# Kernel optimization log

Hardware: AMD Instinct MI355X
Metric: run time of the kernel (lower is better)

The kernel has to match this reference:

```python
import jax, jax.numpy as jnp
import numpy as np

N = 50000   # nodes
E = 800000  # edges
V = 10000   # vocab
D = 128     # emb_dim
H = 128     # hidden_dim
C = 10      # num_classes
G = 512     # graphs in batch


def setup_inputs() -> dict:
    key = jax.random.key(0)
    ks = jax.random.split(key, 10)
    return {
        "x_tokens": jax.random.randint(ks[0], (N,), 0, V),
        "edge_index": jax.random.randint(ks[1], (2, E), 0, N),
        "batch": jnp.sort(jax.random.randint(ks[2], (N,), 0, G)),
        "emb": jax.random.normal(ks[3], (V, D), dtype=jnp.float32) * 0.05,
        "w1": jax.random.normal(ks[4], (D, H), dtype=jnp.float32) * 0.05,
        "b1": jax.random.normal(ks[5], (H,), dtype=jnp.float32) * 0.05,
        "w2": jax.random.normal(ks[6], (H, H), dtype=jnp.float32) * 0.05,
        "b2": jax.random.normal(ks[7], (H,), dtype=jnp.float32) * 0.05,
        "lin_w": jax.random.normal(ks[8], (H, C), dtype=jnp.float32) * 0.05,
        "lin_b": jax.random.normal(ks[9], (C,), dtype=jnp.float32) * 0.05,
    }


def _gcn_conv(x, W, b, src, dst, norm):
    # PyG GCNConv: x' = D^{-1/2}(A+I)D^{-1/2} X W + b (self-loops already in src/dst)
    h = x @ W                                  # [N, H]
    msg = h[src] * norm[:, None]               # [E+N, H] gather + scale
    return jax.ops.segment_sum(msg, dst, num_segments=N) + b


def reference(x_tokens, edge_index, batch, emb, w1, b1, w2, b2, lin_w, lin_b):
    # embedding with padding_idx=0 (row 0 forced to zero)
    table = emb * (jnp.arange(V) != 0)[:, None].astype(emb.dtype)
    x = table[x_tokens]                        # [N, D]

    # add self loops, symmetric degree normalization (computed once)
    loops = jnp.arange(N)
    src = jnp.concatenate([edge_index[0], loops])
    dst = jnp.concatenate([edge_index[1], loops])
    deg = jax.ops.segment_sum(jnp.ones_like(dst, dtype=x.dtype), dst, num_segments=N)
    dis = jax.lax.rsqrt(deg)                   # deg >= 1 due to self loops
    norm = dis[src] * dis[dst]                 # [E+N]

    x = jax.nn.relu(_gcn_conv(x, w1, b1, src, dst, norm))
    x = jax.nn.relu(_gcn_conv(x, w2, b2, src, dst, norm))

    # global mean pool over graphs
    sums = jax.ops.segment_sum(x, batch, num_segments=G)          # [G, H]
    cnts = jax.ops.segment_sum(jnp.ones((N,), x.dtype), batch, num_segments=G)
    pooled = sums / jnp.maximum(cnts, 1.0)[:, None]

    return pooled @ lin_w + lin_b              # [G, C]
```

## Files before the change

### kernel.cpp

```cpp
#include <hip/hip_runtime.h>
#include <hip/hip_bf16.h>


typedef unsigned int uint;
typedef unsigned short ushort;
typedef __attribute__((ext_vector_type(8))) short bf16x8;
typedef __attribute__((ext_vector_type(4))) float f32x4;

__device__ inline float bf_lo(uint u) { return __uint_as_float(u << 16); }
__device__ inline float bf_hi(uint u) { return __uint_as_float(u & 0xffff0000u); }
__device__ inline ushort f2bf(float f) {
    uint u = __float_as_uint(f);
    return (ushort)((u + 0x7fffu + ((u >> 16) & 1u)) >> 16);
}
__device__ inline uint pack2bf(float a, float b) {
    return (uint)f2bf(a) | ((uint)f2bf(b) << 16);
}

#define EPB 2048
#define CAP 8192

__global__ __launch_bounds__(256) void init0(int* __restrict__ bcur,
                                             const float* __restrict__ W1,
                                             const float* __restrict__ W2,
                                             ushort* __restrict__ W1t,
                                             ushort* __restrict__ W2t) {
    if (blockIdx.x == 0) {
        bcur[threadIdx.x] = 0;
    } else {
        int i = (blockIdx.x - 1) * 256 + threadIdx.x;
        const float* Ws = (i < 16384) ? W1 : W2;
        ushort* Wd      = (i < 16384) ? W1t : W2t;
        int j = i & 16383;
        int nn = j >> 7, k = j & 127;
        Wd[j] = f2bf(Ws[k * 128 + nn]);
    }
}

__device__ void scatter_body(int* lds,
                             const int* __restrict__ src,
                             const int* __restrict__ dst,
                             int* __restrict__ bcur,
                             uint* __restrict__ bstage,
                             int E, int NB, int bid) {
    int*  lh    = lds;
    int*  lbase = lds + 256;
    int*  gbase = lds + 513;
    int*  lcur  = lds + 769;
    int*  ls    = lds + 1025;
    uint* stage = (uint*)(lds + 1284);
    const int t = threadIdx.x;
    const int base = bid * EPB;
    const int end  = min(E, base + EPB);
    const int tot  = end - base;

    lh[t] = 0;
    __syncthreads();

    uint pk[8]; int bk[8]; int cnt = 0;
    for (int i = base + t; i < end; i += 256) {
        int s = src[i];
        uint d = (uint)dst[i];
        bk[cnt] = (int)(d >> 8);
        pk[cnt] = (uint)s | ((d & 255u) << 24);
        atomicAdd(&lh[bk[cnt]], 1);
        ++cnt;
    }
    __syncthreads();

    if (t < NB && lh[t]) gbase[t] = t * CAP + atomicAdd(&bcur[t], lh[t]);
    {
        int v = lh[t];
        ls[t] = v;
        __syncthreads();
        for (int off = 1; off < 256; off <<= 1) {
            int x = (t >= off) ? ls[t - off] : 0;
            __syncthreads();
            ls[t] += x;
            __syncthreads();
        }
        lbase[t] = ls[t] - v;
        if (t == 255) lbase[256] = ls[255];
        lcur[t] = 0;
    }
    __syncthreads();

    for (int j = 0; j < cnt; ++j) {
        int p = lbase[bk[j]] + atomicAdd(&lcur[bk[j]], 1);
        stage[p] = pk[j];
    }
    __syncthreads();

    for (int i = t; i < tot; i += 256) {
        int lo = 0, hi = 256;
        while (lo + 1 < hi) {
            int mid = (lo + hi) >> 1;
            if (lbase[mid] <= i) lo = mid; else hi = mid;
        }
        bstage[gbase[lo] + (i - lbase[lo])] = stage[i];
    }
}

__device__ void csr_body(int* lds,
                         const uint* __restrict__ bstage,
                         const int* __restrict__ bcur,
                         float* __restrict__ dis,
                         int* __restrict__ rbeg,
                         int* __restrict__ rend,
                         int* __restrict__ csr,
                         int N, int b) {
    int* lh    = lds;
    int* ls    = lds + 256;
    int* lbase = lds + 512;
    int* lcur  = lds + 768;
    const int t = threadIdx.x;
    const int base  = b * CAP;
    const int cntb  = bcur[b];
    const int n0    = b << 8;
    const int nn    = min(256, N - n0);

    lh[t] = 0;
    __syncthreads();
    for (int i = t; i < cntb; i += 256)
        atomicAdd(&lh[bstage[base + i] >> 24], 1);
    __syncthreads();

    const int v = lh[t];
    ls[t] = v;
    __syncthreads();
    for (int off = 1; off < 256; off <<= 1) {
        int x = (t >= off) ? ls[t - off] : 0;
        __syncthreads();
        ls[t] += x;
        __syncthreads();
    }
    lbase[t] = ls[t] - v;
    lcur[t] = 0;
    if (t < nn) {
        dis[n0 + t]  = rsqrtf((float)v + 1.0f);
        rbeg[n0 + t] = base + lbase[t];
        rend[n0 + t] = base + lbase[t] + v;
    }
    __syncthreads();

    for (int i = t; i < cntb; i += 256) {
        uint e = bstage[base + i];
        int dl = (int)(e >> 24);
        int pos = base + lbase[dl] + atomicAdd(&lcur[dl], 1);
        csr[pos] = (int)(e & 0xFFFFFFu);
    }
}

template<bool GATHER, bool SCALE>
__device__ void gemm_body(ushort* wl,
                          const ushort* __restrict__ Xbf,
                          const int* __restrict__ tokens,
                          const float* __restrict__ emb,
                          const ushort* __restrict__ Wt,
                          const float* __restrict__ dis,
                          ushort* __restrict__ Out, int n, int bid) {
    const int tid = threadIdx.x;
    {
        const int row  = tid >> 1;
        const int half = tid & 1;
        const int base = row * 256 + half * 128;
#pragma unroll
        for (int i = 0; i < 8; ++i) {
            int off = base + i * 16;
            uint4 v = *(const uint4*)((const char*)Wt + off);
            int swz = off ^ ((row & 7) << 4);
            *(uint4*)((char*)wl + swz) = v;
        }
    }
    __syncthreads();

    const int w  = tid >> 6;
    const int l  = tid & 63;
    const int lr = l & 15;
    const int lg = l >> 4;
    const int rowBase = bid * 128 + w * 32;

    f32x4 acc[2][8];
#pragma unroll
    for (int s = 0; s < 2; ++s)
#pragma unroll
        for (int ct = 0; ct < 8; ++ct) acc[s][ct] = (f32x4){0.f, 0.f, 0.f, 0.f};

    bf16x8 afrag[2][4];
#pragma unroll
    for (int s = 0; s < 2; ++s) {
        const int row = rowBase + s * 16 + lr;
        if (row < n) {
            if (GATHER) {
                const int tok = tokens[row];
                if (tok != 0) {
                    const float* ep = emb + (size_t)tok * 128;
#pragma unroll
                    for (int kk = 0; kk < 4; ++kk) {
                        const float* q = ep + kk * 32 + lg * 8;
                        float4 lo = *(const float4*)q;
                        float4 hi = *(const float4*)(q + 4);
                        uint4 pk;
                        pk.x = pack2bf(lo.x, lo.y); pk.y = pack2bf(lo.z, lo.w);
                        pk.z = pack2bf(hi.x, hi.y); pk.w = pack2bf(hi.z, hi.w);
                        union { uint4 u; bf16x8 b; } c; c.u = pk;
                        afrag[s][kk] = c.b;
                    }
                } else {
#pragma unroll
                    for (int kk = 0; kk < 4; ++kk) afrag[s][kk] = (bf16x8){0,0,0,0,0,0,0,0};
                }
            } else {
                const ushort* xp = Xbf + (size_t)row * 128;
#pragma unroll
                for (int kk = 0; kk < 4; ++kk)
                    afrag[s][kk] = *(const bf16x8*)(xp + kk * 32 + lg * 8);
            }
        } else {
#pragma unroll
            for (int kk = 0; kk < 4; ++kk) afrag[s][kk] = (bf16x8){0,0,0,0,0,0,0,0};
        }
    }

#pragma unroll
    for (int ct = 0; ct < 8; ++ct) {
#pragma unroll
        for (int kk = 0; kk < 4; ++kk) {
            const int nrow = ct * 16 + lr;
            int off = nrow * 256 + kk * 64 + lg * 16;
            off ^= ((nrow & 7) << 4);
            bf16x8 b = *(const bf16x8*)((const char*)wl + off);
            acc[0][ct] = __builtin_amdgcn_mfma_f32_16x16x32_bf16(afrag[0][kk], b, acc[0][ct], 0, 0, 0);
            acc[1][ct] = __builtin_amdgcn_mfma_f32_16x16x32_bf16(afrag[1][kk], b, acc[1][ct], 0, 0, 0);
        }
    }

#pragma unroll
    for (int s = 0; s < 2; ++s) {
#pragma unroll
        for (int r = 0; r < 4; ++r) {
            const int row = rowBase + s * 16 + lg * 4 + r;
            if (row < n) {
                const float sc = SCALE ? dis[row] : 1.0f;
                ushort* op = Out + (size_t)row * 128 + lr;
#pragma unroll
                for (int ct = 0; ct < 8; ++ct)
                    op[ct * 16] = f2bf(acc[s][ct][r] * sc);
            }
        }
    }
}

__global__ __launch_bounds__(256) void scatter_gemm1_fused(const int* __restrict__ src,
                                                           const int* __restrict__ dst,
                                                           int* __restrict__ bcur,
                                                           uint* __restrict__ bstage,
                                                           const int* __restrict__ tokens,
                                                           const float* __restrict__ emb,
                                                           const ushort* __restrict__ W1t,
                                                           ushort* __restrict__ H,
                                                           int E, int NB, int EB, int N) {
    __shared__ ushort wl[128 * 128];
    const int b = blockIdx.x;
    if (b < EB) {
        scatter_body((int*)wl, src, dst, bcur, bstage, E, NB, b);
    } else {
        gemm_body<true, false>(wl, nullptr, tokens, emb, W1t, nullptr, H, N, b - EB);
    }
}

__global__ __launch_bounds__(256) void csr_poolz(const uint* __restrict__ bstage,
                                                 const int* __restrict__ bcur,
                                                 float* __restrict__ dis,
                                                 int* __restrict__ rbeg,
                                                 int* __restrict__ rend,
                                                 int* __restrict__ csr,
                                                 int4* __restrict__ poolz, int pz4,
                                                 int N, int NB) {
    __shared__ int lds[1024];
    const int b = blockIdx.x;
    if (b < NB) {
        csr_body(lds, bstage, bcur, dis, rbeg, rend, csr, N, b);
    } else {
        int i = (b - NB) * 256 + threadIdx.x;
        if (i < pz4) poolz[i] = make_int4(0, 0, 0, 0);
    }
}

__global__ __launch_bounds__(256) void gemm2_kernel(const ushort* __restrict__ Xbf,
                                                    const ushort* __restrict__ Wt,
                                                    const float* __restrict__ dis,
                                                    ushort* __restrict__ Out, int n) {
    __shared__ ushort wl[128 * 128];
    gemm_body<false, true>(wl, Xbf, nullptr, nullptr, Wt, dis, Out, n, blockIdx.x);
}

__global__ __launch_bounds__(256) void aggregate_w(const ushort* __restrict__ H,
                                                   const float* __restrict__ dis,
                                                   const int* __restrict__ rbeg,
                                                   const int* __restrict__ rend,
                                                   const int* __restrict__ csr,
                                                   const float* __restrict__ bias,
                                                   ushort* __restrict__ Out, int n) {
    const int g = threadIdx.x >> 4;
    const int l = threadIdx.x & 15;
    const int node = blockIdx.x * 16 + g;
    if (node >= n) return;

    const float dn = dis[node];
    const uint4 hq = *(const uint4*)(H + (size_t)node * 128 + l * 8);
    const int e0 = rbeg[node];
    const int e1 = rend[node];

    float s0_=0.f,s1_=0.f,s2_=0.f,s3_=0.f,s4_=0.f,s5_=0.f,s6_=0.f,s7_=0.f;

    int e = e0;
    for (; e + 8 <= e1; e += 8) {
        int a[8];
#pragma unroll
        for (int j = 0; j < 8; ++j) a[j] = csr[e + j];
        float w[8];
#pragma unroll
        for (int j = 0; j < 8; ++j) w[j] = dis[a[j]];
        uint4 h[8];
#pragma unroll
        for (int j = 0; j < 8; ++j) h[j] = *(const uint4*)(H + (size_t)a[j] * 128 + l * 8);
#pragma unroll
        for (int j = 0; j < 8; ++j) {
            s0_ += bf_lo(h[j].x) * w[j]; s1_ += bf_hi(h[j].x) * w[j];
            s2_ += bf_lo(h[j].y) * w[j]; s3_ += bf_hi(h[j].y) * w[j];
            s4_ += bf_lo(h[j].z) * w[j]; s5_ += bf_hi(h[j].z) * w[j];
            s6_ += bf_lo(h[j].w) * w[j]; s7_ += bf_hi(h[j].w) * w[j];
        }
    }
    for (; e + 4 <= e1; e += 4) {
        int a[4];
#pragma unroll
        for (int j = 0; j < 4; ++j) a[j] = csr[e + j];
        float w[4];
#pragma unroll
        for (int j = 0; j < 4; ++j) w[j] = dis[a[j]];
        uint4 h[4];
#pragma unroll
        for (int j = 0; j < 4; ++j) h[j] = *(const uint4*)(H + (size_t)a[j] * 128 + l * 8);
#pragma unroll
        for (int j = 0; j < 4; ++j) {
            s0_ += bf_lo(h[j].x) * w[j]; s1_ += bf_hi(h[j].x) * w[j];
            s2_ += bf_lo(h[j].y) * w[j]; s3_ += bf_hi(h[j].y) * w[j];
            s4_ += bf_lo(h[j].z) * w[j]; s5_ += bf_hi(h[j].z) * w[j];
            s6_ += bf_lo(h[j].w) * w[j]; s7_ += bf_hi(h[j].w) * w[j];
        }
    }
    for (; e < e1; ++e) {
        const int a = csr[e];
        const float w = dis[a];
        const uint4 h = *(const uint4*)(H + (size_t)a * 128 + l * 8);
        s0_ += bf_lo(h.x)*w; s1_ += bf_hi(h.x)*w;
        s2_ += bf_lo(h.y)*w; s3_ += bf_hi(h.y)*w;
        s4_ += bf_lo(h.z)*w; s5_ += bf_hi(h.z)*w;
        s6_ += bf_lo(h.w)*w; s7_ += bf_hi(h.w)*w;
    }

    const float self = dn * dn;
    const float4 bA = *(const float4*)&bias[l * 8];
    const float4 bB = *(const float4*)&bias[l * 8 + 4];
    float o0 = fmaxf(s0_ * dn + bf_lo(hq.x) * self + bA.x, 0.0f);
    float o1 = fmaxf(s1_ * dn + bf_hi(hq.x) * self + bA.y, 0.0f);
    float o2 = fmaxf(s2_ * dn + bf_lo(hq.y) * self + bA.z, 0.0f);
    float o3 = fmaxf(s3_ * dn + bf_hi(hq.y) * self + bA.w, 0.0f);
    float o4 = fmaxf(s4_ * dn + bf_lo(hq.z) * self + bB.x, 0.0f);
    float o5 = fmaxf(s5_ * dn + bf_hi(hq.z) * self + bB.y, 0.0f);
    float o6 = fmaxf(s6_ * dn + bf_lo(hq.w) * self + bB.z, 0.0f);
    float o7 = fmaxf(s7_ * dn + bf_hi(hq.w) * self + bB.w, 0.0f);

    uint4 o;
    o.x = pack2bf(o0, o1); o.y = pack2bf(o2, o3);
    o.z = pack2bf(o4, o5); o.w = pack2bf(o6, o7);
    *(uint4*)(Out + (size_t)node * 128 + l * 8) = o;
}

__global__ __launch_bounds__(256) void aggregate_pool(const ushort* __restrict__ H,
                                                      const float* __restrict__ dis,
                                                      const int* __restrict__ rbeg,
                                                      const int* __restrict__ rend,
                                                      const int* __restrict__ csr,
                                                      const float* __restrict__ bias,
                                                      const int* __restrict__ batch,
                                                      float* __restrict__ pooled,
                                                      int n) {
    const int g = threadIdx.x >> 4;
    const int l = threadIdx.x & 15;
    const int node = blockIdx.x * 16 + g;
    const bool valid = node < n;

    float s0_=0.f,s1_=0.f,s2_=0.f,s3_=0.f,s4_=0.f,s5_=0.f,s6_=0.f,s7_=0.f;
    float dn = 0.f;
    const float4 bA = *(const float4*)&bias[l * 8];
    const float4 bB = *(const float4*)&bias[l * 8 + 4];

    if (valid) {
        dn = dis[node];
        const uint4 hq = *(const uint4*)(H + (size_t)node * 128 + l * 8);
        s0_ = bf_lo(hq.x); s1_ = bf_hi(hq.x);
        s2_ = bf_lo(hq.y); s3_ = bf_hi(hq.y);
        s4_ = bf_lo(hq.z); s5_ = bf_hi(hq.z);
        s6_ = bf_lo(hq.w); s7_ = bf_hi(hq.w);

        const int e0 = rbeg[node];
        const int e1 = rend[node];
        int e = e0;
        for (; e + 8 <= e1; e += 8) {
            int a[8];
#pragma unroll
            for (int j = 0; j < 8; ++j) a[j] = csr[e + j];
            uint4 h[8];
#pragma unroll
            for (int j = 0; j < 8; ++j) h[j] = *(const uint4*)(H + (size_t)a[j] * 128 + l * 8);
#pragma unroll
            for (int j = 0; j < 8; ++j) {
                s0_ += bf_lo(h[j].x); s1_ += bf_hi(h[j].x);
                s2_ += bf_lo(h[j].y); s3_ += bf_hi(h[j].y);
                s4_ += bf_lo(h[j].z); s5_ += bf_hi(h[j].z);
                s6_ += bf_lo(h[j].w); s7_ += bf_hi(h[j].w);
            }
        }
        for (; e + 4 <= e1; e += 4) {
            int a[4];
#pragma unroll
            for (int j = 0; j < 4; ++j) a[j] = csr[e + j];
            uint4 h[4];
#pragma unroll
            for (int j = 0; j < 4; ++j) h[j] = *(const uint4*)(H + (size_t)a[j] * 128 + l * 8);
#pragma unroll
            for (int j = 0; j < 4; ++j) {
                s0_ += bf_lo(h[j].x); s1_ += bf_hi(h[j].x);
                s2_ += bf_lo(h[j].y); s3_ += bf_hi(h[j].y);
                s4_ += bf_lo(h[j].z); s5_ += bf_hi(h[j].z);
                s6_ += bf_lo(h[j].w); s7_ += bf_hi(h[j].w);
            }
        }
        for (; e < e1; ++e) {
            const uint4 h = *(const uint4*)(H + (size_t)csr[e] * 128 + l * 8);
            s0_ += bf_lo(h.x); s1_ += bf_hi(h.x);
            s2_ += bf_lo(h.y); s3_ += bf_hi(h.y);
            s4_ += bf_lo(h.z); s5_ += bf_hi(h.z);
            s6_ += bf_lo(h.w); s7_ += bf_hi(h.w);
        }
    }

    const float o0 = fmaxf(s0_ * dn + bA.x, 0.0f);
    const float o1 = fmaxf(s1_ * dn + bA.y, 0.0f);
    const float o2 = fmaxf(s2_ * dn + bA.z, 0.0f);
    const float o3 = fmaxf(s3_ * dn + bA.w, 0.0f);
    const float o4 = fmaxf(s4_ * dn + bB.x, 0.0f);
    const float o5 = fmaxf(s5_ * dn + bB.y, 0.0f);
    const float o6 = fmaxf(s6_ * dn + bB.z, 0.0f);
    const float o7 = fmaxf(s7_ * dn + bB.w, 0.0f);

    __shared__ float x3[16][128];
    __shared__ int bv[16];
    if (valid) {
        float4 va, vb;
        va.x = o0; va.y = o1; va.z = o2; va.w = o3;
        vb.x = o4; vb.y = o5; vb.z = o6; vb.w = o7;
        *(float4*)&x3[g][l * 8]     = va;
        *(float4*)&x3[g][l * 8 + 4] = vb;
        if (l == 0) bv[g] = batch[node];
    } else if (l == 0) {
        bv[g] = -1;
    }
    __syncthreads();
    const int t = threadIdx.x;
    if (t < 128) {
        int cur = bv[0];
        float run = 0.0f;
        for (int r = 0; r < 16; ++r) {
            const int b = bv[r];
            if (b < 0) break;
            if (b != cur) {
                if (run != 0.0f) atomicAdd(&pooled[(size_t)cur * 128 + t], run);
                cur = b; run = 0.0f;
            }
            run += x3[r][t];
        }
        if (cur >= 0 && run != 0.0f) atomicAdd(&pooled[(size_t)cur * 128 + t], run);
    }
}

__global__ __launch_bounds__(128) void pool_finalize(const float* __restrict__ pooled,
                                                     const int* __restrict__ batch,
                                                     const float* __restrict__ lw,
                                                     const float* __restrict__ lb,
                                                     float* __restrict__ out, int n) {
    const int g = blockIdx.x;
    const int t = threadIdx.x;
    int lo = 0, hi = n;
    while (lo < hi) { int mid = (lo + hi) >> 1; if (batch[mid] < g) lo = mid + 1; else hi = mid; }
    const int s = lo;
    hi = n;
    while (lo < hi) { int mid = (lo + hi) >> 1; if (batch[mid] < g + 1) lo = mid + 1; else hi = mid; }
    const float c = fmaxf((float)(lo - s), 1.0f);

    __shared__ float pl[128];
    pl[t] = pooled[(size_t)g * 128 + t] / c;
    __syncthreads();
    if (t < 10) {
        float acc = lb[t];
#pragma unroll 16
        for (int d = 0; d < 128; ++d) acc += pl[d] * lw[d * 10 + t];
        out[g * 10 + t] = acc;
    }
}

extern "C" void kernel_launch(void* const* d_in, const int* in_sizes, int n_in,
                              void* d_out, int out_size, void* d_ws, size_t ws_size,
                              hipStream_t stream) {
    const int*   tokens = (const int*)d_in[0];
    const int*   eidx   = (const int*)d_in[1];
    const int*   batch  = (const int*)d_in[2];
    const float* emb    = (const float*)d_in[3];
    const float* w1     = (const float*)d_in[4];
    const float* b1     = (const float*)d_in[5];
    const float* w2     = (const float*)d_in[6];
    const float* b2     = (const float*)d_in[7];
    const float* lw     = (const float*)d_in[8];
    const float* lbv    = (const float*)d_in[9];

    const int N = in_sizes[0];
    const int E = in_sizes[1] / 2;
    const int G = out_size / 10;
    const int* src = eidx;
    const int* dst = eidx + E;
    const int NB = (N + 255) >> 8;
    const int GB = (N + 127) / 128;

    char* p = (char*)d_ws;
    auto alloc = [&](size_t bytes) { void* r = (void*)p; p += (bytes + 255) & ~(size_t)255; return r; };
    float*  dis    = (float*)alloc((size_t)N * 4);
    int*    rbeg   = (int*)  alloc((size_t)N * 4);
    int*    rend   = (int*)  alloc((size_t)N * 4);
    int*    bcur   = (int*)  alloc(256 * 4);
    float*  pooled = (float*)alloc((size_t)G * 128 * 4);
    uint*   bstage = (uint*) alloc((size_t)NB * CAP * 4);
    int*    csr    = (int*)  alloc((size_t)NB * CAP * 4);
    ushort* W1t    = (ushort*)alloc(16384 * 2);
    ushort* W2t    = (ushort*)alloc(16384 * 2);
    ushort* A      = (ushort*)alloc((size_t)N * 128 * 2);
    ushort* B      = (ushort*)alloc((size_t)N * 128 * 2);

    const int PZ4 = (G * 128) / 4;
    const int PZB = (PZ4 + 255) / 256;
    const int EB  = (E + EPB - 1) / EPB;

    init0<<<129, 256, 0, stream>>>(bcur, w1, w2, W1t, W2t);
    scatter_gemm1_fused<<<EB + GB, 256, 0, stream>>>(src, dst, bcur, bstage,
                                                     tokens, emb, W1t, A, E, NB, EB, N);
    csr_poolz<<<NB + PZB, 256, 0, stream>>>(bstage, bcur, dis, rbeg, rend, csr,
                                            (int4*)pooled, PZ4, N, NB);
    aggregate_w<<<(N + 15) / 16, 256, 0, stream>>>(A, dis, rbeg, rend, csr, b1, B, N);
    gemm2_kernel<<<GB, 256, 0, stream>>>(B, W2t, dis, A, N);
    aggregate_pool<<<(N + 15) / 16, 256, 0, stream>>>(A, dis, rbeg, rend, csr, b2, batch, pooled, N);
    pool_finalize<<<G, 128, 0, stream>>>(pooled, batch, lw, lbv, (float*)d_out, N);
}
```

Baseline: 135.4 us.

## Fuse layer-1 aggregation with layer-2 GEMM via LDS-staged MFMA tile

Merges the first GCN aggregation and the second-layer dense transform into one kernel. Each block aggregates 16 nodes, writes the bf16 results to a swizzled shared tile, then runs 16x16x32 MFMAs against W2t read directly from global and scales by dis before storing. This removes a kernel launch and the write-then-reread of the intermediate hidden matrix. In exchange, every block re-reads the full W2 from global/L2 without LDS staging, and the output stores are scattered 2-byte writes rather than vectorized ones.

Measured after the change: 132.7 us, median of 2. 1.02x faster.

```diff
diff --git a/kernel.cpp b/kernel.cpp
--- a/kernel.cpp
+++ b/kernel.cpp
@@ -287,96 +287,139 @@
     }
 }
 
-__global__ __launch_bounds__(256) void gemm2_kernel(const ushort* __restrict__ Xbf,
-                                                    const ushort* __restrict__ Wt,
-                                                    const float* __restrict__ dis,
-                                                    ushort* __restrict__ Out, int n) {
-    __shared__ ushort wl[128 * 128];
-    gemm_body<false, true>(wl, Xbf, nullptr, nullptr, Wt, dis, Out, n, blockIdx.x);
-}
-
-__global__ __launch_bounds__(256) void aggregate_w(const ushort* __restrict__ H,
-                                                   const float* __restrict__ dis,
-                                                   const int* __restrict__ rbeg,
-                                                   const int* __restrict__ rend,
-                                                   const int* __restrict__ csr,
-                                                   const float* __restrict__ bias,
-                                                   ushort* __restrict__ Out, int n) {
+__global__ __launch_bounds__(256) void agg1_gemm2(const ushort* __restrict__ H,
+                                                  const float* __restrict__ dis,
+                                                  const int* __restrict__ rbeg,
+                                                  const int* __restrict__ rend,
+                                                  const int* __restrict__ csr,
+                                                  const float* __restrict__ bias,
+                                                  const ushort* __restrict__ W2t,
+                                                  ushort* __restrict__ Hs2,
+                                                  int n) {
     const int g = threadIdx.x >> 4;
     const int l = threadIdx.x & 15;
     const int node = blockIdx.x * 16 + g;
-    if (node >= n) return;
-
-    const float dn = dis[node];
-    const uint4 hq = *(const uint4*)(H + (size_t)node * 128 + l * 8);
-    const int e0 = rbeg[node];
-    const int e1 = rend[node];
+    const bool valid = node < n;
 
     float s0_=0.f,s1_=0.f,s2_=0.f,s3_=0.f,s4_=0.f,s5_=0.f,s6_=0.f,s7_=0.f;
-
-    int e = e0;
-    for (; e + 8 <= e1; e += 8) {
-        int a[8];
-#pragma unroll
-        for (int j = 0; j < 8; ++j) a[j] = csr[e + j];
-        float w[8];
-#pragma unroll
-        for (int j = 0; j < 8; ++j) w[j] = dis[a[j]];
-        uint4 h[8];
-#pragma unroll
-        for (int j = 0; j < 8; ++j) h[j] = *(const uint4*)(H + (size_t)a[j] * 128 + l * 8);
-#pragma unroll
-        for (int j = 0; j < 8; ++j) {
-            s0_ += bf_lo(h[j].x) * w[j]; s1_ += bf_hi(h[j].x) * w[j];
-            s2_ += bf_lo(h[j].y) * w[j]; s3_ += bf_hi(h[j].y) * w[j];
-            s4_ += bf_lo(h[j].z) * w[j]; s5_ += bf_hi(h[j].z) * w[j];
-            s6_ += bf_lo(h[j].w) * w[j]; s7_ += bf_hi(h[j].w) * w[j];
-        }
-    }
-    for (; e + 4 <= e1; e += 4) {
-        int a[4];
-#pragma unroll
-        for (int j = 0; j < 4; ++j) a[j] = csr[e + j];
-        float w[4];
-#pragma unroll
-        for (int j = 0; j < 4; ++j) w[j] = dis[a[j]];
-        uint4 h[4];
-#pragma unroll
-        for (int j = 0; j < 4; ++j) h[j] = *(const uint4*)(H + (size_t)a[j] * 128 + l * 8);
-#pragma unroll
-        for (int j = 0; j < 4; ++j) {
-            s0_ += bf_lo(h[j].x) * w[j]; s1_ += bf_hi(h[j].x) * w[j];
-            s2_ += bf_lo(h[j].y) * w[j]; s3_ += bf_hi(h[j].y) * w[j];
-            s4_ += bf_lo(h[j].z) * w[j]; s5_ += bf_hi(h[j].z) * w[j];
-            s6_ += bf_lo(h[j].w) * w[j]; s7_ += bf_hi(h[j].w) * w[j];
-        }
-    }
-    for (; e < e1; ++e) {
-        const int a = csr[e];
-        const float w = dis[a];
-        const uint4 h = *(const uint4*)(H + (size_t)a * 128 + l * 8);
-        s0_ += bf_lo(h.x)*w; s1_ += bf_hi(h.x)*w;
-        s2_ += bf_lo(h.y)*w; s3_ += bf_hi(h.y)*w;
-        s4_ += bf_lo(h.z)*w; s5_ += bf_hi(h.z)*w;
-        s6_ += bf_lo(h.w)*w; s7_ += bf_hi(h.w)*w;
-    }
-
-    const float self = dn * dn;
+    float dn = 0.f;
     const float4 bA = *(const float4*)&bias[l * 8];
     const float4 bB = *(const float4*)&bias[l * 8 + 4];
-    float o0 = fmaxf(s0_ * dn + bf_lo(hq.x) * self + bA.x, 0.0f);
-    float o1 = fmaxf(s1_ * dn + bf_hi(hq.x) * self + bA.y, 0.0f);
-    float o2 = fmaxf(s2_ * dn + bf_lo(hq.y) * self + bA.z, 0.0f);
-    float o3 = fmaxf(s3_ * dn + bf_hi(hq.y) * self + bA.w, 0.0f);
-    float o4 = fmaxf(s4_ * dn + bf_lo(hq.z) * self + bB.x, 0.0f);
-    float o5 = fmaxf(s5_ * dn + bf_hi(hq.z) * self + bB.y, 0.0f);
-    float o6 = fmaxf(s6_ * dn + bf_lo(hq.w) * self + bB.z, 0.0f);
-    float o7 = fmaxf(s7_ * dn + bf_hi(hq.w) * self + bB.w, 0.0f);
-
+    float hx0=0.f,hx1=0.f,hx2=0.f,hx3=0.f,hx4=0.f,hx5=0.f,hx6=0.f,hx7=0.f;
+
+    if (valid) {
+        dn = dis[node];
+        const uint4 hq = *(const uint4*)(H + (size_t)node * 128 + l * 8);
+        hx0 = bf_lo(hq.x); hx1 = bf_hi(hq.x);
+        hx2 = bf_lo(hq.y); hx3 = bf_hi(hq.y);
+        hx4 = bf_lo(hq.z); hx5 = bf_hi(hq.z);
+        hx6 = bf_lo(hq.w); hx7 = bf_hi(hq.w);
+
+        const int e0 = rbeg[node];
+        const int e1 = rend[node];
+        int e = e0;
+        for (; e + 8 <= e1; e += 8) {
+            int a[8];
+#pragma unroll
+            for (int j = 0; j < 8; ++j) a[j] = csr[e + j];
+            float w[8];
+#pragma unroll
+            for (int j = 0; j < 8; ++j) w[j] = dis[a[j]];
+            uint4 h[8];
+#pragma unroll
+            for (int j = 0; j < 8; ++j) h[j] = *(const uint4*)(H + (size_t)a[j] * 128 + l * 8);
+#pragma unroll
+            for (int j = 0; j < 8; ++j) {
+                s0_ += bf_lo(h[j].x) * w[j]; s1_ += bf_hi(h[j].x) * w[j];
+                s2_ += bf_lo(h[j].y) * w[j]; s3_ += bf_hi(h[j].y) * w[j];
+                s4_ += bf_lo(h[j].z) * w[j]; s5_ += bf_hi(h[j].z) * w[j];
+                s6_ += bf_lo(h[j].w) * w[j]; s7_ += bf_hi(h[j].w) * w[j];
+            }
+        }
+        for (; e + 4 <= e1; e += 4) {
+            int a[4];
+#pragma unroll
+            for (int j = 0; j < 4; ++j) a[j] = csr[e + j];
+            float w[4];
+#pragma unroll
+            for (int j = 0; j < 4; ++j) w[j] = dis[a[j]];
+            uint4 h[4];
+#pragma unroll
+            for (int j = 0; j < 4; ++j) h[j] = *(const uint4*)(H + (size_t)a[j] * 128 + l * 8);
+#pragma unroll
+            for (int j = 0; j < 4; ++j) {
+                s0_ += bf_lo(h[j].x) * w[j]; s1_ += bf_hi(h[j].x) * w[j];
+                s2_ += bf_lo(h[j].y) * w[j]; s3_ += bf_hi(h[j].y) * w[j];
+                s4_ += bf_lo(h[j].z) * w[j]; s5_ += bf_hi(h[j].z) * w[j];
+                s6_ += bf_lo(h[j].w) * w[j]; s7_ += bf_hi(h[j].w) * w[j];
+            }
+        }
+        for (; e < e1; ++e) {
+            const int a = csr[e];
+            const float w = dis[a];
+            const uint4 h = *(const uint4*)(H + (size_t)a * 128 + l * 8);
+            s0_ += bf_lo(h.x)*w; s1_ += bf_hi(h.x)*w;
+            s2_ += bf_lo(h.y)*w; s3_ += bf_hi(h.y)*w;
+            s4_ += bf_lo(h.z)*w; s5_ += bf_hi(h.z)*w;
+            s6_ += bf_lo(h.w)*w; s7_ += bf_hi(h.w)*w;
+        }
+    }
+
+    const float self = dn * dn;
     uint4 o;
-    o.x = pack2bf(o0, o1); o.y = pack2bf(o2, o3);
-    o.z = pack2bf(o4, o5); o.w = pack2bf(o6, o7);
-    *(uint4*)(Out + (size_t)node * 128 + l * 8) = o;
+    o.x = pack2bf(fmaxf(s0_ * dn + hx0 * self + bA.x, 0.0f),
+                  fmaxf(s1_ * dn + hx1 * self + bA.y, 0.0f));
+    o.y = pack2bf(fmaxf(s2_ * dn + hx2 * self + bA.z, 0.0f),
+                  fmaxf(s3_ * dn + hx3 * self + bA.w, 0.0f));
+    o.z = pack2bf(fmaxf(s4_ * dn + hx4 * self + bB.x, 0.0f),
+                  fmaxf(s5_ * dn + hx5 * self + bB.y, 0.0f));
+    o.w = pack2bf(fmaxf(s6_ * dn + hx6 * self + bB.z, 0.0f),
+                  fmaxf(s7_ * dn + hx7 * self + bB.w, 0.0f));
+
+    __shared__ ushort x2[16 * 128];
+    {
+        int boff = (g << 8) + (l << 4);
+        boff ^= (g & 7) << 4;
+        *(uint4*)((char*)x2 + boff) = o;
+    }
+    __syncthreads();
+
+    const int w   = threadIdx.x >> 6;
+    const int l64 = threadIdx.x & 63;
+    const int lr  = l64 & 15;
+    const int lg  = l64 >> 4;
+
+    bf16x8 afr[4];
+#pragma unroll
+    for (int kk = 0; kk < 4; ++kk) {
+        int roff = (lr << 8) + (kk << 6) + (lg << 4);
+        roff ^= (lr & 7) << 4;
+        afr[kk] = *(const bf16x8*)((const char*)x2 + roff);
+    }
+
+    f32x4 acc[2];
+    acc[0] = (f32x4){0.f, 0.f, 0.f, 0.f};
+    acc[1] = (f32x4){0.f, 0.f, 0.f, 0.f};
+#pragma unroll
+    for (int ci = 0; ci < 2; ++ci) {
+        const int ct = (w << 1) | ci;
+#pragma unroll
+        for (int kk = 0; kk < 4; ++kk) {
+            bf16x8 b = *(const bf16x8*)(W2t + (size_t)(ct * 16 + lr) * 128 + kk * 32 + lg * 8);
+            acc[ci] = __builtin_amdgcn_mfma_f32_16x16x32_bf16(afr[kk], b, acc[ci], 0, 0, 0);
+        }
+    }
+
+#pragma unroll
+    for (int r = 0; r < 4; ++r) {
+        const int row = blockIdx.x * 16 + lg * 4 + r;
+        if (row < n) {
+            const float sc = dis[row];
+            ushort* op = Hs2 + (size_t)row * 128 + lr;
+            op[(w * 2) * 16]     = f2bf(acc[0][r] * sc);
+            op[(w * 2 + 1) * 16] = f2bf(acc[1][r] * sc);
+        }
+    }
 }
 
 __global__ __launch_bounds__(256) void aggregate_pool(const ushort* __restrict__ H,
@@ -557,8 +600,7 @@
                                                      tokens, emb, W1t, A, E, NB, EB, N);
     csr_poolz<<<NB + PZB, 256, 0, stream>>>(bstage, bcur, dis, rbeg, rend, csr,
                                             (int4*)pooled, PZ4, N, NB);
-    aggregate_w<<<(N + 15) / 16, 256, 0, stream>>>(A, dis, rbeg, rend, csr, b1, B, N);
-    gemm2_kernel<<<GB, 256, 0, stream>>>(B, W2t, dis, A, N);
-    aggregate_pool<<<(N + 15) / 16, 256, 0, stream>>>(A, dis, rbeg, rend, csr, b2, batch, pooled, N);
+    agg1_gemm2<<<(N + 15) / 16, 256, 0, stream>>>(A, dis, rbeg, rend, csr, b1, W2t, B, N);
+    aggregate_pool<<<(N + 15) / 16, 256, 0, stream>>>(B, dis, rbeg, rend, csr, b2, batch, pooled, N);
     pool_finalize<<<G, 128, 0, stream>>>(pooled, batch, lw, lbv, (float*)d_out, N);
 }
```
